# Performance work log

Hardware: AMD Instinct MI355X
Metric: run time of the kernel (lower is better)

The kernel has to match this reference:

```python
import jax, jax.numpy as jnp
import numpy as np
import math

# ---- hyperparameters taken verbatim from the source losses ----
NSAMPLE_REP = 20      # ballquery nsample in get_repulsion_loss
RADIUS_REP = 0.07     # ballquery radius in get_repulsion_loss
H_REP = 0.03          # kernel bandwidth h
PERCENTAGES = (0.004, 0.008, 0.01, 0.012, 0.016)
UNI_RADIUS = 1.0


def _gather(p, idx):
    # p: [B, N, 3], idx: [B, ...] int -> [B, ..., 3]  (pointops.grouping/gathering)
    return jax.vmap(lambda pts, i: pts[i])(p, idx)


def _ballquery(radius, nsample, q, p):
    # pointops.ballquery: for each query, first `nsample` point indices within
    # radius, padded with the first found index. q:[B,M,3], p:[B,N,3] -> [B,M,nsample]
    d = jnp.sum((q[:, :, None, :] - p[:, None, :, :]) ** 2, -1)  # [B,M,N]
    N = p.shape[1]
    keys = jnp.where(d <= radius * radius,
                     jnp.arange(N, dtype=jnp.int32)[None, None, :], N)
    idx = jnp.sort(keys, axis=-1)[..., :nsample]
    return jnp.where(idx >= N, idx[..., :1], idx)  # pad misses with first hit


def _fps(pcd, npoint):
    # pointops.furthestsampling on [B,N,3] -> [B,npoint] int32
    B, N, _ = pcd.shape
    bidx = jnp.arange(B)

    def step(carry, _):
        dist, far = carry                         # [B,N], [B]
        pt = pcd[bidx, far]                       # [B,3]
        d = jnp.sum((pcd - pt[:, None, :]) ** 2, -1)
        dist = jnp.minimum(dist, d)
        nxt = jnp.argmax(dist, -1).astype(jnp.int32)
        return (dist, nxt), far

    init = (jnp.full((B, N), 1e10, pcd.dtype), jnp.zeros((B,), jnp.int32))
    _, idxs = jax.lax.scan(step, init, None, length=npoint)
    return idxs.T  # [B, npoint]


def _repulsion_loss(pred):
    # pred: [B, N, 3]
    idx = _ballquery(RADIUS_REP, NSAMPLE_REP, pred, pred)   # [B,N,20], detached ints
    g = _gather(pred, idx) - pred[:, :, None, :]            # [B,N,20,3]
    dists = jnp.sum(g * g, -1)                              # [B,N,20]
    vals, _ = jax.lax.top_k(-dists, 5)                      # 5 smallest sq-dists
    d5 = jnp.maximum(-vals[:, :, 1:], 0.0)                  # drop self, ReLU
    ds = jnp.sqrt(d5)
    w = jnp.exp(-d5 / (H_REP * H_REP))
    return jnp.mean(RADIUS_REP - ds * w)


def _uniform_loss(pcd):
    # pcd: [B, N, 3]
    N = pcd.shape[1]
    npoint = int(N * 0.05)
    # FPS is called with identical args for every percentage -> compute once.
    fps_idx = _fps(jax.lax.stop_gradient(pcd), npoint)
    new_xyz = _gather(pcd, fps_idx)                          # [B,npoint,3]
    loss = jnp.zeros((), pcd.dtype)
    for p in PERCENTAGES:
        nsample = int(N * p)
        r = math.sqrt(p * UNI_RADIUS)
        disk_area = math.pi * UNI_RADIUS ** 2 * p / nsample
        expect_len = math.sqrt(2 * disk_area / 1.732)
        idx = _ballquery(r, nsample, new_xyz, pcd)           # [B,npoint,nsample]
        grouped = _gather(pcd, idx).reshape(-1, nsample, 3)  # [B*npoint,nsample,3]
        # knn_point(2, grouped, grouped): pairwise sq-dists inside each disk
        d = jnp.sum((grouped[:, :, None, :] - grouped[:, None, :, :]) ** 2, -1)
        vals, _ = jax.lax.top_k(-d, 2)
        ud = -vals[:, :, 1:]                                  # nearest non-self sqdist
        ud = jnp.sqrt(jnp.abs(ud + 1e-8))
        ud = jnp.mean(ud, -1)
        ud = (ud - expect_len) ** 2 / (expect_len + 1e-8)
        loss = loss + jnp.mean(ud) * (p * 100.0) ** 2
    return loss / len(PERCENTAGES)


def setup_inputs() -> dict:
    key = jax.random.key(0)
    # refined upsampled cloud: B=4, r*N = 4*2048 = 8192 points in [-1,1]^3
    pcd = jax.random.uniform(key, (4, 8192, 3), jnp.float32) * 2.0 - 1.0
    return {"pcd": pcd}


def reference(pcd):
    return jnp.stack([_uniform_loss(pcd), _repulsion_loss(pcd)])
```

## Files before the change

### kernel.cpp

```cpp
#include <hip/hip_runtime.h>
#include <hip/hip_bf16.h>
#include <cmath>
#include <cfloat>

#define BATCH 4
#define NPTS 8192
#define NPOINT 409
#define NBALLS (BATCH * NPOINT)
#define REP_NS 20
#define REP_SEG 8
#define SEG_LEN (NPTS / REP_SEG)
#define REP_TASKS 512
#define NTASKS (REP_TASKS + NBALLS)
#define NWORKERS 252
#define NBLOCKS (BATCH + NWORKERS)

#define UW 96
#define UH (8 * UW)

#define WS_FPS_OFF 0
#define WS_REP_OFF 8192
#define WS_UNI_OFF 12288
#define WS_CNT_OFF 25600

typedef float v2f __attribute__((ext_vector_type(2)));

struct UniParams {
  float  thr[5];
  float  e[5];
  float  eden[5];
  int    ns[5];
};

template <int CTRL>
__device__ __forceinline__ unsigned dpp_max_u32(unsigned v) {
  const unsigned o = (unsigned)__builtin_amdgcn_update_dpp(
      0, (int)v, CTRL, 0xf, 0xf, true);
  return o > v ? o : v;
}

__device__ __forceinline__ void ins5(float v, float& t0, float& t1, float& t2,
                                     float& t3, float& t4) {
  if (v < t4) {
    t4 = v;
    if (t4 < t3) { float tmp = t3; t3 = t4; t4 = tmp; }
    if (t3 < t2) { float tmp = t2; t2 = t3; t3 = tmp; }
    if (t2 < t1) { float tmp = t1; t1 = t2; t2 = tmp; }
    if (t1 < t0) { float tmp = t0; t0 = t1; t1 = tmp; }
  }
}

__device__ __forceinline__ float rep_term(float d) {
  d = fmaxf(d, 0.0f);
  return 0.07f - sqrtf(d) * expf(-(d / 0.0009f));
}

__global__ __launch_bounds__(512, 2) void fused_kernel(const float* __restrict__ pcd,
                                                       int* __restrict__ fps_idx,
                                                       double* __restrict__ rep_part,
                                                       double* __restrict__ uni_part,
                                                       int* __restrict__ counter,
                                                       float* __restrict__ out,
                                                       UniParams up, float rep_thr) {
  const int tid = threadIdx.x;
  const int lane = tid & 63;
  const int w = tid >> 6;
  extern __shared__ float smem[];

  __shared__ unsigned long long s_key[2][8];
  __shared__ float s_t5[REP_SEG][64][5];
  __shared__ float s_d0[REP_SEG][64];
  __shared__ int   s_cnt[REP_SEG][64];
  __shared__ float wx[8][UW], wy[8][UW], wz[8][UW], wd[8][UW];
  __shared__ int   s_wcnt[8];
  __shared__ float FX[UH], FY[UH], FZ[UH], FD[UH];
  __shared__ float CX[5][131], CY[5][131], CZ[5][131];
  __shared__ double dpart[8], rpart[8];
  __shared__ int s_task, s_qidx, s_last;

  if (blockIdx.x < BATCH) {
    const int b = blockIdx.x;
    const float* P = pcd + b * NPTS * 3;
    float* X = smem;
    float* Y = smem + NPTS;
    float* Z = smem + 2 * NPTS;

    for (int i = tid; i < NPTS; i += 512) {
      X[i] = P[i * 3 + 0];
      Y[i] = P[i * 3 + 1];
      Z[i] = P[i * 3 + 2];
    }

    v2f px[8], py[8], pz[8], dist[8];
    const int base = tid * 16;
#pragma unroll
    for (int k = 0; k < 8; k++) {
      const int i0 = (base + 2 * k) * 3;
      const int i1 = (base + 2 * k + 1) * 3;
      px[k] = (v2f){P[i0 + 0], P[i1 + 0]};
      py[k] = (v2f){P[i0 + 1], P[i1 + 1]};
      pz[k] = (v2f){P[i0 + 2], P[i1 + 2]};
      dist[k] = (v2f){1e10f, 1e10f};
    }
#pragma unroll
    for (int k = 0; k < 8; k++) {
      asm volatile("" : "+v"(px[k]), "+v"(py[k]), "+v"(pz[k]));
    }

    __syncthreads();

    int far = 0;
    float fx = X[0], fy = Y[0], fz = Z[0];
    for (int s = 0; s < NPOINT; s++) {
      if (tid == 0) {
        __hip_atomic_store(&fps_idx[b * NPOINT + s], far,
                           __ATOMIC_RELAXED, __HIP_MEMORY_SCOPE_AGENT);
      }

      const v2f fxv = (v2f){fx, fx};
      const v2f fyv = (v2f){fy, fy};
      const v2f fzv = (v2f){fz, fz};
#pragma unroll
      for (int k = 0; k < 8; k++) {
#pragma clang fp contract(off)
        const v2f dx = px[k] - fxv;
        const v2f dy = py[k] - fyv;
        const v2f dz = pz[k] - fzv;
        const v2f d  = (dx * dx + dy * dy) + dz * dz;
        dist[k].x = fminf(dist[k].x, d.x);
        dist[k].y = fminf(dist[k].y, d.y);
      }

      const float m0 = fmaxf(fmaxf(dist[0].x, dist[0].y),
                             fmaxf(dist[1].x, dist[1].y));
      const float m1 = fmaxf(fmaxf(dist[2].x, dist[2].y),
                             fmaxf(dist[3].x, dist[3].y));
      const float m2 = fmaxf(fmaxf(dist[4].x, dist[4].y),
                             fmaxf(dist[5].x, dist[5].y));
      const float m3 = fmaxf(fmaxf(dist[6].x, dist[6].y),
                             fmaxf(dist[7].x, dist[7].y));
      const float tmax = fmaxf(fmaxf(m0, m1), fmaxf(m2, m3));

      const unsigned tb = __float_as_uint(tmax);
      unsigned rb = tb;
      rb = dpp_max_u32<0x111>(rb);
      rb = dpp_max_u32<0x112>(rb);
      rb = dpp_max_u32<0x114>(rb);
      rb = dpp_max_u32<0x118>(rb);
      rb = dpp_max_u32<0x142>(rb);
      rb = dpp_max_u32<0x143>(rb);
      const unsigned wb = (unsigned)__builtin_amdgcn_readlane((int)rb, 63);

      const unsigned long long hit = __ballot(tb == wb);
      const int par = s & 1;
      if (tb == wb && (hit & ((1ull << lane) - 1ull)) == 0ull) {
        const float wv = __uint_as_float(wb);
        int li = 0;
#pragma unroll
        for (int j = 15; j >= 0; j--) {
          const float v = (j & 1) ? dist[j >> 1].y : dist[j >> 1].x;
          li = (v == wv) ? j : li;
        }
        const unsigned bidx = (unsigned)(base + li);
        s_key[par][w] = ((unsigned long long)wb << 32) |
                        (unsigned long long)(0xFFFFFFFFu - bidx);
      }
      __syncthreads();

      unsigned long long kbk = s_key[par][0];
#pragma unroll
      for (int w2 = 1; w2 < 8; w2++) {
        const unsigned long long kk = s_key[par][w2];
        if (kk > kbk) kbk = kk;
      }
      far = (int)(0xFFFFFFFFu - (unsigned)(kbk & 0xFFFFFFFFull));
      fx = X[far];
      fy = Y[far];
      fz = Z[far];
    }
  } else {
    const double wj_tab[5] = {0.16 / (5.0 * 1636.0 * 32.0),
                              0.64 / (5.0 * 1636.0 * 65.0),
                              1.0  / (5.0 * 1636.0 * 81.0),
                              1.44 / (5.0 * 1636.0 * 98.0),
                              2.56 / (5.0 * 1636.0 * 131.0)};

    while (true) {
      __syncthreads();
      if (tid == 0) s_task = atomicAdd(counter, 1);
      __syncthreads();
      const int t = s_task;
      if (t >= NTASKS) break;

      if (t < REP_TASKS) {
        const int b = t >> 7;
        const int q = ((t & 127) << 6) + lane;
        const float* P = pcd + b * NPTS * 3;

        const float qx = P[q * 3 + 0], qy = P[q * 3 + 1], qz = P[q * 3 + 2];

        int cnt = 0;
        float d0 = 0.0f;
        float t0 = FLT_MAX, t1 = FLT_MAX, t2 = FLT_MAX, t3 = FLT_MAX, t4 = FLT_MAX;

        const int wu = __builtin_amdgcn_readfirstlane(w);
        const float* S = P + wu * SEG_LEN * 3;
#pragma unroll 4
        for (int i = 0; i < SEG_LEN; i++) {
          const float x = S[i * 3 + 0];
          const float y = S[i * 3 + 1];
          const float z = S[i * 3 + 2];
          const float dx = qx - x, dy = qy - y, dz = qz - z;
          const float d = dx * dx + dy * dy + dz * dz;
          if (d <= rep_thr && cnt < REP_NS) {
            if (cnt == 0) d0 = d;
            ins5(d, t0, t1, t2, t3, t4);
            cnt++;
          }
        }

        s_t5[w][lane][0] = t0; s_t5[w][lane][1] = t1; s_t5[w][lane][2] = t2;
        s_t5[w][lane][3] = t3; s_t5[w][lane][4] = t4;
        s_d0[w][lane] = d0;
        s_cnt[w][lane] = cnt;
        __syncthreads();

        if (w == 0) {
          int total = 0;
          float fd0 = 0.0f;
          int first_seen = 0;
          float n0 = FLT_MAX, n1 = FLT_MAX, n2 = FLT_MAX, n3 = FLT_MAX, n4 = FLT_MAX;
#pragma unroll
          for (int sg = 0; sg < REP_SEG; sg++) {
            const int c = s_cnt[sg][lane];
            if (c > 0 && !first_seen) { fd0 = s_d0[sg][lane]; first_seen = 1; }
            total += c;
#pragma unroll
            for (int j = 0; j < 5; j++) ins5(s_t5[sg][lane][j], n0, n1, n2, n3, n4);
          }

          if (total > REP_NS) {
            int c2 = 0;
            n0 = FLT_MAX; n1 = FLT_MAX; n2 = FLT_MAX; n3 = FLT_MAX; n4 = FLT_MAX;
            for (int i = 0; i < NPTS && c2 < REP_NS; i++) {
              const float dx = qx - P[i * 3 + 0];
              const float dy = qy - P[i * 3 + 1];
              const float dz = qz - P[i * 3 + 2];
              const float d = dx * dx + dy * dy + dz * dz;
              if (d <= rep_thr) { ins5(d, n0, n1, n2, n3, n4); c2++; }
            }
          } else {
            for (int c = total; c < REP_NS; c++) ins5(fd0, n0, n1, n2, n3, n4);
          }

          float sum = rep_term(n1) + rep_term(n2) + rep_term(n3) + rep_term(n4);
#pragma unroll
          for (int off = 32; off >= 1; off >>= 1) sum += __shfl_down(sum, off);
          if (lane == 0) rep_part[t] = (double)sum;
        }
      } else {
        const int ball = t - REP_TASKS;
        const int b = ball / NPOINT;
        const float* P = pcd + b * NPTS * 3;

        if (tid == 0) {
          int v = __hip_atomic_load(&fps_idx[ball], __ATOMIC_RELAXED,
                                    __HIP_MEMORY_SCOPE_AGENT);
          while (v < 0) {
            __builtin_amdgcn_s_sleep(32);
            v = __hip_atomic_load(&fps_idx[ball], __ATOMIC_RELAXED,
                                  __HIP_MEMORY_SCOPE_AGENT);
          }
          s_qidx = v;
        }
        __syncthreads();
        const int qidx = s_qidx;
        const float qx = P[qidx * 3 + 0], qy = P[qidx * 3 + 1], qz = P[qidx * 3 + 2];

        int wcnt = 0;
        const float* S = P + w * 1024 * 3;
        for (int it = 0; it < 16; it++) {
          const int j = it * 64 + lane;
          const float x = S[j * 3 + 0];
          const float y = S[j * 3 + 1];
          const float z = S[j * 3 + 2];
          const float dx = qx - x, dy = qy - y, dz = qz - z;
          const float d = dx * dx + dy * dy + dz * dz;
          const bool hitp = (d <= up.thr[4]);
          const unsigned long long m = __ballot(hitp);
          if (hitp) {
            const int pos = wcnt + __popcll(m & ((1ull << lane) - 1ull));
            if (pos < UW) {
              wx[w][pos] = x; wy[w][pos] = y; wz[w][pos] = z; wd[w][pos] = d;
            }
          }
          wcnt += __popcll(m);
        }
        if (lane == 0) s_wcnt[w] = min(wcnt, UW);
        __syncthreads();

        int off = 0;
#pragma unroll
        for (int w2 = 0; w2 < 8; w2++) {
          if (w2 == w) break;
          off += s_wcnt[w2];
        }
        for (int i = lane; i < s_wcnt[w]; i += 64) {
          FX[off + i] = wx[w][i]; FY[off + i] = wy[w][i];
          FZ[off + i] = wz[w][i]; FD[off + i] = wd[w][i];
        }
        __syncthreads();
        int c = 0;
#pragma unroll
        for (int w2 = 0; w2 < 8; w2++) c += s_wcnt[w2];

        double local = 0.0;
        if (w < 5) {
          const int jp = w;
          const float thr = up.thr[jp];
          const int nsj = up.ns[jp];

          int cnt2 = 0;
          for (int bse = 0; bse < c; bse += 64) {
            const int e = bse + lane;
            const bool pred = (e < c) && (FD[e] <= thr);
            const unsigned long long m = __ballot(pred);
            if (pred) {
              const int pos = cnt2 + __popcll(m & ((1ull << lane) - 1ull));
              if (pos < nsj) {
                CX[jp][pos] = FX[e]; CY[jp][pos] = FY[e]; CZ[jp][pos] = FZ[e];
              }
            }
            cnt2 += __popcll(m);
          }
          const int cj = min(cnt2, nsj);
          const int pads = nsj - cj;
          const int istart = (pads > 0) ? 1 : 0;

          if (pads > 0 && lane == 0) {
            const float ud = sqrtf(fabsf(1e-8f));
            const float dd = ud - up.e[jp];
            const float tt = (dd * dd) / up.eden[jp];
            local += (double)tt * wj_tab[jp] * (double)(pads + 1);
          }

          for (int r = istart + lane; r < cj; r += 64) {
            const float xi = CX[jp][r], yi = CY[jp][r], zi = CZ[jp][r];
            float mm = FLT_MAX;
            for (int e2 = 0; e2 < cj; e2++) {
              if (e2 == r) continue;
              const float dx = xi - CX[jp][e2];
              const float dy = yi - CY[jp][e2];
              const float dz = zi - CZ[jp][e2];
              const float d = dx * dx + dy * dy + dz * dz;
              if (d < mm) mm = d;
            }
            const float ud = sqrtf(fabsf(mm + 1e-8f));
            const float dd = ud - up.e[jp];
            const float tt = (dd * dd) / up.eden[jp];
            local += (double)tt * wj_tab[jp];
          }
        }

#pragma unroll
        for (int o = 32; o >= 1; o >>= 1) local += __shfl_down(local, o);
        if (lane == 0) dpart[w] = local;
        __syncthreads();
        if (tid == 0) {
          double u = 0.0;
#pragma unroll
          for (int w2 = 0; w2 < 8; w2++) u += dpart[w2];
          uni_part[ball] = u;
        }
      }
    }
  }

  __syncthreads();
  if (tid == 0) {
    __threadfence();
    const int old = __hip_atomic_fetch_add(counter + 1, 1, __ATOMIC_ACQ_REL,
                                           __HIP_MEMORY_SCOPE_AGENT);
    s_last = (old == NBLOCKS - 1) ? 1 : 0;
    if (s_last) __threadfence();
  }
  __syncthreads();
  if (s_last) {
    double u = 0.0, r = 0.0;
    for (int i = tid; i < NBALLS; i += 512) u += uni_part[i];
    for (int i = tid; i < REP_TASKS; i += 512) r += rep_part[i];
#pragma unroll
    for (int o = 32; o >= 1; o >>= 1) {
      u += __shfl_down(u, o);
      r += __shfl_down(r, o);
    }
    if (lane == 0) { dpart[w] = u; rpart[w] = r; }
    __syncthreads();
    if (tid == 0) {
      double us = 0.0, rs = 0.0;
#pragma unroll
      for (int w2 = 0; w2 < 8; w2++) { us += dpart[w2]; rs += rpart[w2]; }
      out[0] = (float)us;
      out[1] = (float)(rs * (1.0 / 131072.0));
    }
  }
}

extern "C" void kernel_launch(void* const* d_in, const int* in_sizes, int n_in,
                              void* d_out, int out_size, void* d_ws, size_t ws_size,
                              hipStream_t stream) {
  (void)in_sizes; (void)n_in; (void)out_size; (void)ws_size;
  const float* pcd = (const float*)d_in[0];
  float* out = (float*)d_out;
  int*    fps      = (int*)((char*)d_ws + WS_FPS_OFF);
  double* rep_part = (double*)((char*)d_ws + WS_REP_OFF);
  double* uni_part = (double*)((char*)d_ws + WS_UNI_OFF);
  int*    counter  = (int*)((char*)d_ws + WS_CNT_OFF);

  const float rep_thr = (float)(0.07 * 0.07);

  UniParams up;
  const double ps[5] = {0.004, 0.008, 0.01, 0.012, 0.016};
  for (int j = 0; j < 5; j++) {
    const int ns = (int)(8192.0 * ps[j]);
    const double r = sqrt(ps[j]);
    up.thr[j] = (float)(r * r);
    const double disk = M_PI * ps[j] / (double)ns;
    const double el = sqrt(2.0 * disk / 1.732);
    up.e[j] = (float)el;
    up.eden[j] = (float)(el + 1e-8);
    up.ns[j] = ns;
  }

  hipMemsetAsync(fps, 0xFF, NBALLS * sizeof(int), stream);
  hipMemsetAsync(counter, 0, 2 * sizeof(int), stream);

  static const int kDynLds = NPTS * 3 * (int)sizeof(float);
  (void)hipFuncSetAttribute((const void*)fused_kernel,
                            hipFuncAttributeMaxDynamicSharedMemorySize, kDynLds);

  fused_kernel<<<NBLOCKS, 512, kDynLds, stream>>>(pcd, fps, rep_part, uni_part,
                                                  counter, out, up, rep_thr);
}
```

Baseline: 413.9 us.

## Use static worker task striding, merge memsets, and hand-write packed FPS distance

Worker blocks now stride over tasks statically instead of claiming them through an atomic counter. The done counter is placed inside the memset region and initialised to -1, so a single memset replaces two and the last-block test becomes NBLOCKS-2. The FPS distance step is written as inline packed add/mul assembly using negated centre coordinates, and the 8-way key reduction becomes a max tree. This removes one memset launch and the atomic traffic per task, at the cost of losing dynamic load balance across uneven tasks.

```diff
diff --git a/kernel.cpp b/kernel.cpp
--- a/kernel.cpp
+++ b/kernel.cpp
@@ -19,9 +19,9 @@
 #define UH (8 * UW)
 
 #define WS_FPS_OFF 0
+#define WS_DONE_OFF 6544
 #define WS_REP_OFF 8192
 #define WS_UNI_OFF 12288
-#define WS_CNT_OFF 25600
 
 typedef float v2f __attribute__((ext_vector_type(2)));
 
@@ -37,6 +37,27 @@
   const unsigned o = (unsigned)__builtin_amdgcn_update_dpp(
       0, (int)v, CTRL, 0xf, 0xf, true);
   return o > v ? o : v;
+}
+
+__device__ __forceinline__ v2f sqdist_pk(v2f px, v2f py, v2f pz,
+                                         v2f nfx, v2f nfy, v2f nfz) {
+  v2f dx, dy, dz, d;
+  asm("v_pk_add_f32 %0, %4, %7\n\t"
+      "v_pk_add_f32 %1, %5, %8\n\t"
+      "v_pk_add_f32 %2, %6, %9\n\t"
+      "v_pk_mul_f32 %0, %0, %0\n\t"
+      "v_pk_mul_f32 %1, %1, %1\n\t"
+      "v_pk_mul_f32 %2, %2, %2\n\t"
+      "v_pk_add_f32 %3, %0, %1\n\t"
+      "v_pk_add_f32 %3, %3, %2"
+      : "=&v"(dx), "=&v"(dy), "=&v"(dz), "=&v"(d)
+      : "v"(px), "v"(py), "v"(pz), "v"(nfx), "v"(nfy), "v"(nfz));
+  return d;
+}
+
+__device__ __forceinline__ unsigned long long umax64(unsigned long long a,
+                                                     unsigned long long b) {
+  return a > b ? a : b;
 }
 
 __device__ __forceinline__ void ins5(float v, float& t0, float& t1, float& t2,
@@ -59,7 +80,7 @@
                                                        int* __restrict__ fps_idx,
                                                        double* __restrict__ rep_part,
                                                        double* __restrict__ uni_part,
-                                                       int* __restrict__ counter,
+                                                       int* __restrict__ done,
                                                        float* __restrict__ out,
                                                        UniParams up, float rep_thr) {
   const int tid = threadIdx.x;
@@ -76,7 +97,7 @@
   __shared__ float FX[UH], FY[UH], FZ[UH], FD[UH];
   __shared__ float CX[5][131], CY[5][131], CZ[5][131];
   __shared__ double dpart[8], rpart[8];
-  __shared__ int s_task, s_qidx, s_last;
+  __shared__ int s_qidx, s_last;
 
   if (blockIdx.x < BATCH) {
     const int b = blockIdx.x;
@@ -117,16 +138,12 @@
                            __ATOMIC_RELAXED, __HIP_MEMORY_SCOPE_AGENT);
       }
 
-      const v2f fxv = (v2f){fx, fx};
-      const v2f fyv = (v2f){fy, fy};
-      const v2f fzv = (v2f){fz, fz};
+      const v2f nfx = (v2f){-fx, -fx};
+      const v2f nfy = (v2f){-fy, -fy};
+      const v2f nfz = (v2f){-fz, -fz};
 #pragma unroll
       for (int k = 0; k < 8; k++) {
-#pragma clang fp contract(off)
-        const v2f dx = px[k] - fxv;
-        const v2f dy = py[k] - fyv;
-        const v2f dz = pz[k] - fzv;
-        const v2f d  = (dx * dx + dy * dy) + dz * dz;
+        const v2f d = sqdist_pk(px[k], py[k], pz[k], nfx, nfy, nfz);
         dist[k].x = fminf(dist[k].x, d.x);
         dist[k].y = fminf(dist[k].y, d.y);
       }
@@ -167,30 +184,28 @@
       }
       __syncthreads();
 
-      unsigned long long kbk = s_key[par][0];
-#pragma unroll
-      for (int w2 = 1; w2 < 8; w2++) {
-        const unsigned long long kk = s_key[par][w2];
-        if (kk > kbk) kbk = kk;
-      }
+      const unsigned long long k0 = s_key[par][0], k1 = s_key[par][1];
+      const unsigned long long k2 = s_key[par][2], k3 = s_key[par][3];
+      const unsigned long long k4 = s_key[par][4], k5 = s_key[par][5];
+      const unsigned long long k6 = s_key[par][6], k7 = s_key[par][7];
+      const unsigned long long kbk =
+          umax64(umax64(umax64(k0, k1), umax64(k2, k3)),
+                 umax64(umax64(k4, k5), umax64(k6, k7)));
       far = (int)(0xFFFFFFFFu - (unsigned)(kbk & 0xFFFFFFFFull));
       fx = X[far];
       fy = Y[far];
       fz = Z[far];
     }
   } else {
+    const int wk = blockIdx.x - BATCH;
     const double wj_tab[5] = {0.16 / (5.0 * 1636.0 * 32.0),
                               0.64 / (5.0 * 1636.0 * 65.0),
                               1.0  / (5.0 * 1636.0 * 81.0),
                               1.44 / (5.0 * 1636.0 * 98.0),
                               2.56 / (5.0 * 1636.0 * 131.0)};
 
-    while (true) {
+    for (int t = wk; t < NTASKS; t += NWORKERS) {
       __syncthreads();
-      if (tid == 0) s_task = atomicAdd(counter, 1);
-      __syncthreads();
-      const int t = s_task;
-      if (t >= NTASKS) break;
 
       if (t < REP_TASKS) {
         const int b = t >> 7;
@@ -379,9 +394,9 @@
   __syncthreads();
   if (tid == 0) {
     __threadfence();
-    const int old = __hip_atomic_fetch_add(counter + 1, 1, __ATOMIC_ACQ_REL,
+    const int old = __hip_atomic_fetch_add(done, 1, __ATOMIC_ACQ_REL,
                                            __HIP_MEMORY_SCOPE_AGENT);
-    s_last = (old == NBLOCKS - 1) ? 1 : 0;
+    s_last = (old == NBLOCKS - 2) ? 1 : 0;
     if (s_last) __threadfence();
   }
   __syncthreads();
@@ -413,9 +428,9 @@
   const float* pcd = (const float*)d_in[0];
   float* out = (float*)d_out;
   int*    fps      = (int*)((char*)d_ws + WS_FPS_OFF);
+  int*    done     = (int*)((char*)d_ws + WS_DONE_OFF);
   double* rep_part = (double*)((char*)d_ws + WS_REP_OFF);
   double* uni_part = (double*)((char*)d_ws + WS_UNI_OFF);
-  int*    counter  = (int*)((char*)d_ws + WS_CNT_OFF);
 
   const float rep_thr = (float)(0.07 * 0.07);
 
@@ -432,13 +447,12 @@
     up.ns[j] = ns;
   }
 
-  hipMemsetAsync(fps, 0xFF, NBALLS * sizeof(int), stream);
-  hipMemsetAsync(counter, 0, 2 * sizeof(int), stream);
+  hipMemsetAsync(fps, 0xFF, WS_DONE_OFF + sizeof(int), stream);
 
   static const int kDynLds = NPTS * 3 * (int)sizeof(float);
   (void)hipFuncSetAttribute((const void*)fused_kernel,
                             hipFuncAttributeMaxDynamicSharedMemorySize, kDynLds);
 
   fused_kernel<<<NBLOCKS, 512, kDynLds, stream>>>(pcd, fps, rep_part, uni_part,
-                                                  counter, out, up, rep_thr);
-}
+                                                  done, out, up, rep_thr);
+}
```

Measured after the change: 454.8 us. 9.9% more time.
